# Kernel optimization log

Measured on AMD Instinct MI355X. Metric: run time of the kernel, lower is better.

## Reference

```python
import jax, jax.numpy as jnp
import numpy as np

H = 1024
E = 8
TOP_K = 2
B, S = 4, 2048


def setup_inputs() -> dict:
    key = jax.random.key(0)
    ks = jax.random.split(key, 8)
    scale = 0.02
    return {
        "x": jax.random.normal(ks[0], (B, S, H), dtype=jnp.float32),
        "router_w": jax.random.normal(ks[1], (H, E), dtype=jnp.float32) * scale,
        "router_b": jnp.zeros((E,), dtype=jnp.float32),
        "w1": jax.random.normal(ks[2], (E, H, 4 * H), dtype=jnp.float32) * scale,
        "b1": jnp.zeros((E, 4 * H), dtype=jnp.float32),
        "w2": jax.random.normal(ks[3], (E, 4 * H, H), dtype=jnp.float32) * scale,
        "b2": jnp.zeros((E, H), dtype=jnp.float32),
    }


def reference(x, router_w, router_b, w1, b1, w2, b2):
    b, s, h = x.shape
    n_exp = w1.shape[0]
    x_flat = x.reshape(-1, h)  # [T, H]
    T = x_flat.shape[0]

    # Router: softmax then top-k, renormalize top-k probs (matches torch code).
    logits = x_flat @ router_w + router_b            # [T, E]
    probs = jax.nn.softmax(logits, axis=-1)
    top_values, top_indices = jax.lax.top_k(probs, TOP_K)  # [T, k]
    top_values = top_values / jnp.sum(top_values, axis=-1, keepdims=True)

    # Per-token combine weight for each expert (0 if token not routed there).
    combine = jnp.zeros((T, n_exp), dtype=x.dtype)
    combine = combine.at[jnp.arange(T)[:, None], top_indices].add(top_values)  # [T, E]

    # Loop over the small fixed expert set; masked combine weights zero out
    # contributions from unrouted tokens, matching the gather/scatter original.
    out = jnp.zeros_like(x_flat)
    for e in range(n_exp):
        hmid = jax.nn.gelu(x_flat @ w1[e] + b1[e], approximate=False)  # [T, 4H]
        y = hmid @ w2[e] + b2[e]                                       # [T, H]
        out = out + combine[:, e:e + 1] * y
    return out.reshape(b, s, h)
```

## Files before the change

### kernel.cpp

```cpp
#include <hip/hip_runtime.h>
#include <hip/hip_bf16.h>
#include <math.h>

#define TT 8192
#define HD 1024
#define FHD 4096
#define NE 8
#define NTMAX 136

typedef short s16x8 __attribute__((ext_vector_type(8)));
typedef float f32x4 __attribute__((ext_vector_type(4)));
using bf16 = __hip_bfloat16;
typedef unsigned int u32;

#define OFF_COUNTS 0
#define OFF_DONE   32
#define OFF_CURSOR 64
#define OFF_OFFS   128
#define OFF_E0     256
#define OFF_E1     (OFF_E0 + 4*TT)
#define OFF_W0     (OFF_E1 + 4*TT)
#define OFF_W1     (OFF_W0 + 4*TT)
#define OFF_S0     (OFF_W1 + 4*TT)
#define OFF_S1     (OFF_S0 + 4*TT)
#define OFF_TID    (OFF_S1 + 4*TT)
#define OFF_TW     (OFF_TID + 8*TT)
#define OFF_TMR    (OFF_TW + 8*TT)
#define OFF_TME    (OFF_TMR + 4*144)
#define OFF_TMN    (OFF_TME + 4*144)
#define OFF_XBF    (OFF_TMN + 64)
#define OFF_W1T    (OFF_XBF + 2*TT*HD)
#define OFF_W2T    (OFF_W1T + 2*NE*HD*FHD)
#define OFF_HMID   (OFF_W2T + 2*NE*HD*FHD)
#define OFF_YS     (OFF_HMID + (size_t)2*(2*TT)*FHD)

__device__ __forceinline__ void gload_lds16(const void* g, void* l) {
    __builtin_amdgcn_global_load_lds(
        (const __attribute__((address_space(1))) u32*)g,
        (__attribute__((address_space(3))) u32*)l, 16, 0, 0);
}

__global__ __launch_bounds__(256) void prep_kernel(
        const float* __restrict__ x, const float* __restrict__ rw, const float* __restrict__ rb,
        const float* __restrict__ w1, const float* __restrict__ w2,
        bf16* __restrict__ xbf, bf16* __restrict__ w1t, bf16* __restrict__ w2t,
        int* __restrict__ e0a, int* __restrict__ e1a,
        float* __restrict__ w0a, float* __restrict__ w1a,
        int* __restrict__ counts, int* __restrict__ done,
        int* __restrict__ offs, int* __restrict__ cursor,
        int* __restrict__ tmr, int* __restrict__ tme, int* __restrict__ tmn) {
    __shared__ float tile[64][65];
    int bid = blockIdx.x;
    int tid = threadIdx.x;
    if (bid < 16384) {
        const float* in; bf16* out; int R, C, rem;
        if (bid < 8192) { in = w1; out = w1t; R = HD;  C = FHD; rem = bid; }
        else            { in = w2; out = w2t; R = FHD; C = HD;  rem = bid - 8192; }
        int rt = R >> 6, ct = C >> 6;
        int e = rem / (rt * ct);
        int rem2 = rem % (rt * ct);
        int r0 = (rem2 / ct) << 6, c0 = (rem2 % ct) << 6;
        const float* ine = in + (size_t)e * R * C;
        bf16* oute = out + (size_t)e * R * C;
#pragma unroll
        for (int i = 0; i < 4; ++i) {
            int lin = tid + i * 256;
            int r = lin >> 4, cg = lin & 15;
            float4 v = *reinterpret_cast<const float4*>(&ine[(size_t)(r0 + r) * C + c0 + cg * 4]);
            tile[r][cg * 4 + 0] = v.x; tile[r][cg * 4 + 1] = v.y;
            tile[r][cg * 4 + 2] = v.z; tile[r][cg * 4 + 3] = v.w;
        }
        __syncthreads();
#pragma unroll
        for (int i = 0; i < 4; ++i) {
            int lin = tid + i * 256;
            int n = lin >> 4, kg = lin & 15;
            bf16 h[4];
            h[0] = __float2bfloat16(tile[kg * 4 + 0][n]);
            h[1] = __float2bfloat16(tile[kg * 4 + 1][n]);
            h[2] = __float2bfloat16(tile[kg * 4 + 2][n]);
            h[3] = __float2bfloat16(tile[kg * 4 + 3][n]);
            *reinterpret_cast<uint2*>(&oute[(size_t)(c0 + n) * R + r0 + kg * 4]) =
                *reinterpret_cast<uint2*>(h);
        }
        return;
    }
    int rbid = bid - 16384;
    int wid = tid >> 6, lane = tid & 63;
    int t = rbid * 4 + wid;
    const float* xp = x + (size_t)t * HD + lane * 16;
    float xv[16];
#pragma unroll
    for (int j = 0; j < 4; ++j) {
        float4 v = *reinterpret_cast<const float4*>(&xp[j * 4]);
        xv[4 * j] = v.x; xv[4 * j + 1] = v.y; xv[4 * j + 2] = v.z; xv[4 * j + 3] = v.w;
    }
    {
        bf16 hv[16];
#pragma unroll
        for (int j = 0; j < 16; ++j) hv[j] = __float2bfloat16(xv[j]);
        uint4* dst = reinterpret_cast<uint4*>(&xbf[(size_t)t * HD + lane * 16]);
        dst[0] = reinterpret_cast<uint4*>(hv)[0];
        dst[1] = reinterpret_cast<uint4*>(hv)[1];
    }
    float acc[8] = {0.f, 0.f, 0.f, 0.f, 0.f, 0.f, 0.f, 0.f};
    const float* rp = rw + (size_t)(lane * 16) * NE;
#pragma unroll
    for (int hh = 0; hh < 16; ++hh) {
        float4 r0 = *reinterpret_cast<const float4*>(&rp[hh * 8]);
        float4 r1 = *reinterpret_cast<const float4*>(&rp[hh * 8 + 4]);
        acc[0] += xv[hh] * r0.x; acc[1] += xv[hh] * r0.y;
        acc[2] += xv[hh] * r0.z; acc[3] += xv[hh] * r0.w;
        acc[4] += xv[hh] * r1.x; acc[5] += xv[hh] * r1.y;
        acc[6] += xv[hh] * r1.z; acc[7] += xv[hh] * r1.w;
    }
#pragma unroll
    for (int e = 0; e < 8; ++e) {
#pragma unroll
        for (int off = 32; off > 0; off >>= 1) acc[e] += __shfl_xor(acc[e], off, 64);
    }
    if (lane == 0) {
        float lg[8];
#pragma unroll
        for (int e = 0; e < 8; ++e) lg[e] = acc[e] + rb[e];
        int a = 0;
#pragma unroll
        for (int e = 1; e < 8; ++e) if (lg[e] > lg[a]) a = e;
        int b = (a == 0) ? 1 : 0;
#pragma unroll
        for (int e = 0; e < 8; ++e) if (e != a && e != b && lg[e] > lg[b]) b = e;
        float wa = 1.0f / (1.0f + expf(lg[b] - lg[a]));
        float wb = 1.0f / (1.0f + expf(lg[a] - lg[b]));
        e0a[t] = a; e1a[t] = b; w0a[t] = wa; w1a[t] = wb;
        atomicAdd(&counts[a], 1);
        atomicAdd(&counts[b], 1);
    }
    __syncthreads();
    __shared__ int lastFlag;
    if (tid == 0) {
        __threadfence();
        lastFlag = (atomicAdd(done, 1) == 2047) ? 1 : 0;
    }
    __syncthreads();
    if (!lastFlag) return;
    __threadfence();
    __shared__ int cbase[NE + 1], tbase[NE + 1];
    if (tid == 0) {
        int s = 0, ntt = 0;
        for (int e = 0; e < NE; ++e) {
            int c = atomicAdd(&counts[e], 0);
            cbase[e] = s; tbase[e] = ntt;
            s += c; ntt += (c + 127) >> 7;
        }
        cbase[NE] = s; tbase[NE] = ntt;
        tmn[0] = ntt;
        offs[NE] = s;
    }
    __syncthreads();
    if (tid < NE) { offs[tid] = cbase[tid]; cursor[tid] = cbase[tid]; }
    if (tid < NTMAX) {
        int ntt = tbase[NE];
        if (tid < ntt) {
            int e = 0;
            while (tbase[e + 1] <= tid) ++e;
            tmr[tid] = cbase[e] + ((tid - tbase[e]) << 7);
            tme[tid] = e;
        } else { tmr[tid] = 0; tme[tid] = 0; }
    }
}

__global__ __launch_bounds__(256) void scatter_kernel(const int* __restrict__ e0a, const int* __restrict__ e1a,
        const float* __restrict__ w0a, const float* __restrict__ w1a,
        int* __restrict__ cursor, int* __restrict__ tid_arr, float* __restrict__ tw_arr,
        int* __restrict__ slot0, int* __restrict__ slot1) {
    int t = blockIdx.x * 256 + threadIdx.x;
    int s0 = atomicAdd(&cursor[e0a[t]], 1);
    tid_arr[s0] = t; tw_arr[s0] = w0a[t]; slot0[t] = s0;
    int s1 = atomicAdd(&cursor[e1a[t]], 1);
    tid_arr[s1] = t; tw_arr[s1] = w1a[t]; slot1[t] = s1;
}

__global__ __launch_bounds__(256) void gemm1_kernel(const bf16* __restrict__ xbf, const bf16* __restrict__ w1t,
        const float* __restrict__ b1, const int* __restrict__ offs,
        const int* __restrict__ tid_arr, bf16* __restrict__ hmid,
        const int* __restrict__ tmr, const int* __restrict__ tme, const int* __restrict__ tmn) {
    __shared__ bf16 As[128 * 32];
    __shared__ bf16 Bs[128 * 32];
    __shared__ int toks[128];
    int nwg = gridDim.x;
    int orig = blockIdx.x;
    int wg = (orig & 7) * (nwg >> 3) + (orig >> 3);
    int nt = wg / NTMAX;
    int tidx = wg % NTMAX;
    if (tidx >= tmn[0]) return;
    int e = tme[tidx];
    int row0 = tmr[tidx];
    int s1 = offs[e + 1];
    int n0 = nt * 128;
    int tid = threadIdx.x;
    if (tid < 128) { int s = row0 + tid; toks[tid] = tid_arr[(s < s1) ? s : (s1 - 1)]; }
    __syncthreads();
    int lane = tid & 63, w = tid >> 6;
    int wrow = (w >> 1) * 64, wcol = (w & 1) * 64;
    int lr = lane & 15, lk = (lane >> 4) * 8;
    int srow = lane >> 2, seg = lane & 3;
    int tokA0 = toks[w * 32 + srow];
    int tokA1 = toks[w * 32 + 16 + srow];
    const bf16* w1e = w1t + (size_t)e * FHD * HD;
    const bf16* bsrc0 = w1e + (size_t)(n0 + w * 32 + srow) * HD + seg * 8;
    const bf16* bsrc1 = w1e + (size_t)(n0 + w * 32 + 16 + srow) * HD + seg * 8;
    const bf16* asrc0 = xbf + (size_t)tokA0 * HD + seg * 8;
    const bf16* asrc1 = xbf + (size_t)tokA1 * HD + seg * 8;
    bf16* aDst0 = &As[(w * 32) * 32];
    bf16* aDst1 = &As[(w * 32 + 16) * 32];
    bf16* bDst0 = &Bs[(w * 32) * 32];
    bf16* bDst1 = &Bs[(w * 32 + 16) * 32];
    f32x4 acc[4][4] = {};
    for (int k0 = 0; k0 < HD; k0 += 32) {
        gload_lds16(asrc0 + k0, aDst0);
        gload_lds16(asrc1 + k0, aDst1);
        gload_lds16(bsrc0 + k0, bDst0);
        gload_lds16(bsrc1 + k0, bDst1);
        __syncthreads();
        s16x8 aF[4], bF[4];
#pragma unroll
        for (int m = 0; m < 4; ++m) aF[m] = *reinterpret_cast<const s16x8*>(&As[(wrow + m * 16 + lr) * 32 + lk]);
#pragma unroll
        for (int n = 0; n < 4; ++n) bF[n] = *reinterpret_cast<const s16x8*>(&Bs[(wcol + n * 16 + lr) * 32 + lk]);
#pragma unroll
        for (int m = 0; m < 4; ++m)
#pragma unroll
            for (int n = 0; n < 4; ++n)
                acc[m][n] = __builtin_amdgcn_mfma_f32_16x16x32_bf16(aF[m], bF[n], acc[m][n], 0, 0, 0);
        __syncthreads();
    }
#pragma unroll
    for (int m = 0; m < 4; ++m) {
#pragma unroll
        for (int n = 0; n < 4; ++n) {
            int col = n0 + wcol + n * 16 + lr;
            float bv = b1[(size_t)e * FHD + col];
#pragma unroll
            for (int r = 0; r < 4; ++r) {
                int row = wrow + m * 16 + (lane >> 4) * 4 + r;
                int slot = row0 + row;
                if (slot < s1) {
                    float v2 = acc[m][n][r] + bv;
                    v2 = 0.5f * v2 * (1.0f + erff(v2 * 0.70710678118f));
                    hmid[(size_t)slot * FHD + col] = __float2bfloat16(v2);
                }
            }
        }
    }
}

__global__ __launch_bounds__(256) void gemm2_kernel(const bf16* __restrict__ hmid, const bf16* __restrict__ w2t,
        const float* __restrict__ b2, const int* __restrict__ offs, float* __restrict__ ys,
        const int* __restrict__ tmr, const int* __restrict__ tme, const int* __restrict__ tmn) {
    __shared__ bf16 As[128 * 32];
    __shared__ bf16 Bs[128 * 32];
    int nwg = gridDim.x;
    int orig = blockIdx.x;
    int wg = (orig & 7) * (nwg >> 3) + (orig >> 3);
    int nt = wg / NTMAX;
    int tidx = wg % NTMAX;
    if (tidx >= tmn[0]) return;
    int e = tme[tidx];
    int row0 = tmr[tidx];
    int s1 = offs[e + 1];
    int n0 = nt * 128;
    int tid = threadIdx.x;
    int lane = tid & 63, w = tid >> 6;
    int wrow = (w >> 1) * 64, wcol = (w & 1) * 64;
    int lr = lane & 15, lk = (lane >> 4) * 8;
    int srow = lane >> 2, seg = lane & 3;
    int ar0 = row0 + w * 32 + srow;      if (ar0 >= s1) ar0 = s1 - 1;
    int ar1 = row0 + w * 32 + 16 + srow; if (ar1 >= s1) ar1 = s1 - 1;
    const bf16* w2e = w2t + (size_t)e * HD * FHD;
    const bf16* bsrc0 = w2e + (size_t)(n0 + w * 32 + srow) * FHD + seg * 8;
    const bf16* bsrc1 = w2e + (size_t)(n0 + w * 32 + 16 + srow) * FHD + seg * 8;
    const bf16* asrc0 = hmid + (size_t)ar0 * FHD + seg * 8;
    const bf16* asrc1 = hmid + (size_t)ar1 * FHD + seg * 8;
    bf16* aDst0 = &As[(w * 32) * 32];
    bf16* aDst1 = &As[(w * 32 + 16) * 32];
    bf16* bDst0 = &Bs[(w * 32) * 32];
    bf16* bDst1 = &Bs[(w * 32 + 16) * 32];
    f32x4 acc[4][4] = {};
    for (int k0 = 0; k0 < FHD; k0 += 32) {
        gload_lds16(asrc0 + k0, aDst0);
        gload_lds16(asrc1 + k0, aDst1);
        gload_lds16(bsrc0 + k0, bDst0);
        gload_lds16(bsrc1 + k0, bDst1);
        __syncthreads();
        s16x8 aF[4], bF[4];
#pragma unroll
        for (int m = 0; m < 4; ++m) aF[m] = *reinterpret_cast<const s16x8*>(&As[(wrow + m * 16 + lr) * 32 + lk]);
#pragma unroll
        for (int n = 0; n < 4; ++n) bF[n] = *reinterpret_cast<const s16x8*>(&Bs[(wcol + n * 16 + lr) * 32 + lk]);
#pragma unroll
        for (int m = 0; m < 4; ++m)
#pragma unroll
            for (int n = 0; n < 4; ++n)
                acc[m][n] = __builtin_amdgcn_mfma_f32_16x16x32_bf16(aF[m], bF[n], acc[m][n], 0, 0, 0);
        __syncthreads();
    }
#pragma unroll
    for (int m = 0; m < 4; ++m) {
#pragma unroll
        for (int n = 0; n < 4; ++n) {
            int col = n0 + wcol + n * 16 + lr;
            float bv = b2[(size_t)e * HD + col];
#pragma unroll
            for (int r = 0; r < 4; ++r) {
                int row = wrow + m * 16 + (lane >> 4) * 4 + r;
                int slot = row0 + row;
                if (slot < s1) ys[(size_t)slot * HD + col] = acc[m][n][r] + bv;
            }
        }
    }
}

__global__ __launch_bounds__(256) void combine_kernel(const float* __restrict__ ys,
        const int* __restrict__ slot0, const int* __restrict__ slot1,
        const float* __restrict__ tw, float* __restrict__ out) {
    int t = blockIdx.x;
    int c = threadIdx.x * 4;
    int sa = slot0[t], sb = slot1[t];
    float wa = tw[sa], wb = tw[sb];
    float4 a = *reinterpret_cast<const float4*>(&ys[(size_t)sa * HD + c]);
    float4 b = *reinterpret_cast<const float4*>(&ys[(size_t)sb * HD + c]);
    float4 o;
    o.x = wa * a.x + wb * b.x; o.y = wa * a.y + wb * b.y;
    o.z = wa * a.z + wb * b.z; o.w = wa * a.w + wb * b.w;
    *reinterpret_cast<float4*>(&out[(size_t)t * HD + c]) = o;
}

extern "C" void kernel_launch(void* const* d_in, const int* in_sizes, int n_in,
                              void* d_out, int out_size, void* d_ws, size_t ws_size,
                              hipStream_t stream) {
    const float* x  = (const float*)d_in[0];
    const float* rw = (const float*)d_in[1];
    const float* rb = (const float*)d_in[2];
    const float* w1 = (const float*)d_in[3];
    const float* b1 = (const float*)d_in[4];
    const float* w2 = (const float*)d_in[5];
    const float* b2 = (const float*)d_in[6];
    float* out = (float*)d_out;
    char* ws = (char*)d_ws;

    int*   counts  = (int*)(ws + OFF_COUNTS);
    int*   done    = (int*)(ws + OFF_DONE);
    int*   cursor  = (int*)(ws + OFF_CURSOR);
    int*   offs    = (int*)(ws + OFF_OFFS);
    int*   e0a     = (int*)(ws + OFF_E0);
    int*   e1a     = (int*)(ws + OFF_E1);
    float* w0a     = (float*)(ws + OFF_W0);
    float* w1a     = (float*)(ws + OFF_W1);
    int*   slot0   = (int*)(ws + OFF_S0);
    int*   slot1   = (int*)(ws + OFF_S1);
    int*   tid_arr = (int*)(ws + OFF_TID);
    float* tw_arr  = (float*)(ws + OFF_TW);
    int*   tmr     = (int*)(ws + OFF_TMR);
    int*   tme     = (int*)(ws + OFF_TME);
    int*   tmn     = (int*)(ws + OFF_TMN);
    bf16*  xbf     = (bf16*)(ws + OFF_XBF);
    bf16*  w1t     = (bf16*)(ws + OFF_W1T);
    bf16*  w2t     = (bf16*)(ws + OFF_W2T);
    bf16*  hmid    = (bf16*)(ws + OFF_HMID);
    float* ys      = (float*)(ws + OFF_YS);

    hipMemsetAsync(counts, 0, 64, stream);

    prep_kernel<<<18432, 256, 0, stream>>>(x, rw, rb, w1, w2, xbf, w1t, w2t,
        e0a, e1a, w0a, w1a, counts, done, offs, cursor, tmr, tme, tmn);
    scatter_kernel<<<TT / 256, 256, 0, stream>>>(e0a, e1a, w0a, w1a, cursor,
        tid_arr, tw_arr, slot0, slot1);
    gemm1_kernel<<<(FHD / 128) * NTMAX, 256, 0, stream>>>(xbf, w1t, b1, offs, tid_arr, hmid, tmr, tme, tmn);
    gemm2_kernel<<<(HD / 128) * NTMAX, 256, 0, stream>>>(hmid, w2t, b2, offs, ys, tmr, tme, tmn);
    combine_kernel<<<TT, 256, 0, stream>>>(ys, slot0, slot1, tw_arr, out);
}
```

Measured before the change: 921.7 us.

## Split weight transpose into separate kernel with async LDS double-buffering

Moves the fp32-to-bf16 weight transpose out of the combined prep kernel into its own kernel. The new kernel uses larger 128x256 tiles, direct global-to-LDS loads with double buffering, and 16-byte coalesced bf16 stores. The router part becomes its own kernel. The aim is to raise bandwidth on the roughly 256MB weight read that dominates preprocessing, at the cost of one extra launch and heavy LDS use per block.

After: 945.9 us. 1.03x slower.

```diff
diff --git a/kernel.cpp b/kernel.cpp
--- a/kernel.cpp
+++ b/kernel.cpp
@@ -40,54 +40,71 @@
         (__attribute__((address_space(3))) u32*)l, 16, 0, 0);
 }
 
-__global__ __launch_bounds__(256) void prep_kernel(
+__global__ __launch_bounds__(512) void transpose_kernel(const float* __restrict__ w1,
+        const float* __restrict__ w2, bf16* __restrict__ w1t, bf16* __restrict__ w2t) {
+    __shared__ float sub[2][32 * 256];
+    __shared__ bf16 btile[256][136];
+    int bid = blockIdx.x;
+    int t = threadIdx.x;
+    const float* in; bf16* out; int K, C, rem;
+    if (bid < 1024) { in = w1; out = w1t; K = HD;  C = FHD; rem = bid; }
+    else            { in = w2; out = w2t; K = FHD; C = HD;  rem = bid - 1024; }
+    int kch = K >> 7, nch = C >> 8;
+    int per = kch * nch;
+    int e = rem / per;
+    int rem2 = rem % per;
+    int k0 = (rem2 / nch) << 7, n0 = (rem2 % nch) << 8;
+    const float* ine = in + (size_t)e * K * C;
+    bf16* oute = out + (size_t)e * K * C;
+    int wv = t >> 6, ln = t & 63;
+    const float* src_base = ine + (size_t)k0 * C + n0 + ln * 4;
+#pragma unroll
+    for (int j = 0; j < 4; ++j)
+        gload_lds16(src_base + (size_t)(j * 8 + wv) * C,
+                    &sub[0][(j * 8 + wv) * 256 + ln * 4]);
+    for (int p = 0; p < 4; ++p) {
+        int cur = p & 1;
+        if (p + 1 < 4) {
+#pragma unroll
+            for (int j = 0; j < 4; ++j)
+                gload_lds16(src_base + (size_t)((p + 1) * 32 + j * 8 + wv) * C,
+                            &sub[cur ^ 1][(j * 8 + wv) * 256 + ln * 4]);
+            asm volatile("s_waitcnt vmcnt(4)" ::: "memory");
+        } else {
+            asm volatile("s_waitcnt vmcnt(0)" ::: "memory");
+        }
+        __builtin_amdgcn_s_barrier();
+        {
+            int n = t & 255, kh = t >> 8;
+            bf16 h[16];
+#pragma unroll
+            for (int i = 0; i < 16; ++i)
+                h[i] = __float2bfloat16(sub[cur][(kh * 16 + i) * 256 + n]);
+            uint4* dst = reinterpret_cast<uint4*>(&btile[n][p * 32 + kh * 16]);
+            dst[0] = reinterpret_cast<uint4*>(h)[0];
+            dst[1] = reinterpret_cast<uint4*>(h)[1];
+        }
+        asm volatile("s_waitcnt lgkmcnt(0)" ::: "memory");
+        __builtin_amdgcn_s_barrier();
+    }
+#pragma unroll
+    for (int step = 0; step < 8; ++step) {
+        int n = step * 32 + (t >> 4), ch = t & 15;
+        uint4 v = *reinterpret_cast<const uint4*>(&btile[n][ch * 8]);
+        *reinterpret_cast<uint4*>(&oute[(size_t)(n0 + n) * K + k0 + ch * 8]) = v;
+    }
+}
+
+__global__ __launch_bounds__(256) void router_kernel(
         const float* __restrict__ x, const float* __restrict__ rw, const float* __restrict__ rb,
-        const float* __restrict__ w1, const float* __restrict__ w2,
-        bf16* __restrict__ xbf, bf16* __restrict__ w1t, bf16* __restrict__ w2t,
-        int* __restrict__ e0a, int* __restrict__ e1a,
+        bf16* __restrict__ xbf, int* __restrict__ e0a, int* __restrict__ e1a,
         float* __restrict__ w0a, float* __restrict__ w1a,
         int* __restrict__ counts, int* __restrict__ done,
         int* __restrict__ offs, int* __restrict__ cursor,
         int* __restrict__ tmr, int* __restrict__ tme, int* __restrict__ tmn) {
-    __shared__ float tile[64][65];
-    int bid = blockIdx.x;
     int tid = threadIdx.x;
-    if (bid < 16384) {
-        const float* in; bf16* out; int R, C, rem;
-        if (bid < 8192) { in = w1; out = w1t; R = HD;  C = FHD; rem = bid; }
-        else            { in = w2; out = w2t; R = FHD; C = HD;  rem = bid - 8192; }
-        int rt = R >> 6, ct = C >> 6;
-        int e = rem / (rt * ct);
-        int rem2 = rem % (rt * ct);
-        int r0 = (rem2 / ct) << 6, c0 = (rem2 % ct) << 6;
-        const float* ine = in + (size_t)e * R * C;
-        bf16* oute = out + (size_t)e * R * C;
-#pragma unroll
-        for (int i = 0; i < 4; ++i) {
-            int lin = tid + i * 256;
-            int r = lin >> 4, cg = lin & 15;
-            float4 v = *reinterpret_cast<const float4*>(&ine[(size_t)(r0 + r) * C + c0 + cg * 4]);
-            tile[r][cg * 4 + 0] = v.x; tile[r][cg * 4 + 1] = v.y;
-            tile[r][cg * 4 + 2] = v.z; tile[r][cg * 4 + 3] = v.w;
-        }
-        __syncthreads();
-#pragma unroll
-        for (int i = 0; i < 4; ++i) {
-            int lin = tid + i * 256;
-            int n = lin >> 4, kg = lin & 15;
-            bf16 h[4];
-            h[0] = __float2bfloat16(tile[kg * 4 + 0][n]);
-            h[1] = __float2bfloat16(tile[kg * 4 + 1][n]);
-            h[2] = __float2bfloat16(tile[kg * 4 + 2][n]);
-            h[3] = __float2bfloat16(tile[kg * 4 + 3][n]);
-            *reinterpret_cast<uint2*>(&oute[(size_t)(c0 + n) * R + r0 + kg * 4]) =
-                *reinterpret_cast<uint2*>(h);
-        }
-        return;
-    }
-    int rbid = bid - 16384;
     int wid = tid >> 6, lane = tid & 63;
-    int t = rbid * 4 + wid;
+    int t = blockIdx.x * 4 + wid;
     const float* xp = x + (size_t)t * HD + lane * 16;
     float xv[16];
 #pragma unroll
@@ -371,8 +388,9 @@
 
     hipMemsetAsync(counts, 0, 64, stream);
 
-    prep_kernel<<<18432, 256, 0, stream>>>(x, rw, rb, w1, w2, xbf, w1t, w2t,
-        e0a, e1a, w0a, w1a, counts, done, offs, cursor, tmr, tme, tmn);
+    router_kernel<<<TT / 4, 256, 0, stream>>>(x, rw, rb, xbf, e0a, e1a, w0a, w1a,
+        counts, done, offs, cursor, tmr, tme, tmn);
+    transpose_kernel<<<2048, 512, 0, stream>>>(w1, w2, w1t, w2t);
     scatter_kernel<<<TT / 256, 256, 0, stream>>>(e0a, e1a, w0a, w1a, cursor,
         tid_arr, tw_arr, slot0, slot1);
     gemm1_kernel<<<(FHD / 128) * NTMAX, 256, 0, stream>>>(xbf, w1t, b1, offs, tid_arr, hmid, tmr, tme, tmn);
```
